# Kernel tuning notes

Measured on AMD Instinct MI355X. Metric: run time of the kernel, lower is better.

## Reference

```python
import jax, jax.numpy as jnp
import numpy as np

N_GAUSS = 1024
IMG = 192
TANFOV = 0.5  # tan(FoV/2), both axes
ZNEAR, ZFAR = 0.01, 100.0

C0 = 0.28209479177387814
C1 = 0.4886025119029199
C2 = (1.0925484305920792, -1.0925484305920792, 0.31539156525252005, -1.0925484305920792, 0.5462742152960396)
C3 = (-0.5900435899266435, 2.890611442640554, -0.4570457994644658, 0.3731763325901154, -0.4570457994644658, 1.445305721320277, -0.5900435899266435)


def _eval_sh3(sh, d):
    # sh: [N,16,3] coeffs, d: [N,3] unit dirs -> clamped rgb [N,3]
    x, y, z = d[:, 0:1], d[:, 1:2], d[:, 2:3]
    xx, yy, zz = x * x, y * y, z * z
    xy, yz, xz = x * y, y * z, x * z
    res = (C0 * sh[:, 0]
           - C1 * y * sh[:, 1] + C1 * z * sh[:, 2] - C1 * x * sh[:, 3]
           + C2[0] * xy * sh[:, 4] + C2[1] * yz * sh[:, 5]
           + C2[2] * (2.0 * zz - xx - yy) * sh[:, 6]
           + C2[3] * xz * sh[:, 7] + C2[4] * (xx - yy) * sh[:, 8]
           + C3[0] * y * (3.0 * xx - yy) * sh[:, 9]
           + C3[1] * xy * z * sh[:, 10]
           + C3[2] * y * (4.0 * zz - xx - yy) * sh[:, 11]
           + C3[3] * z * (2.0 * zz - 3.0 * xx - 3.0 * yy) * sh[:, 12]
           + C3[4] * x * (4.0 * zz - xx - yy) * sh[:, 13]
           + C3[5] * z * (xx - yy) * sh[:, 14]
           + C3[6] * x * (xx - yy - 3.0 * zz) * sh[:, 15])
    return jnp.maximum(res + 0.5, 0.0)


def _quat_to_rot(q):
    r, x, y, z = q[:, 0], q[:, 1], q[:, 2], q[:, 3]
    return jnp.stack([
        1 - 2 * (y * y + z * z), 2 * (x * y - r * z), 2 * (x * z + r * y),
        2 * (x * y + r * z), 1 - 2 * (x * x + z * z), 2 * (y * z - r * x),
        2 * (x * z - r * y), 2 * (y * z + r * x), 1 - 2 * (x * x + y * y),
    ], axis=-1).reshape(-1, 3, 3)


def setup_inputs() -> dict:
    key = jax.random.key(0)
    ks = jax.random.split(key, 6)
    xy = jax.random.uniform(ks[0], (N_GAUSS, 2), minval=-2.0, maxval=2.0)
    z = jax.random.uniform(ks[1], (N_GAUSS, 1), minval=2.0, maxval=10.0)
    means3D = jnp.concatenate([xy, z], axis=1)
    scales = jax.random.uniform(ks[2], (N_GAUSS, 3), minval=0.01, maxval=0.08)
    q = jax.random.normal(ks[3], (N_GAUSS, 4))
    rotations = q / jnp.linalg.norm(q, axis=1, keepdims=True)
    opacities = jax.random.uniform(ks[4], (N_GAUSS, 1), minval=0.1, maxval=0.99)
    shs = jax.random.normal(ks[5], (N_GAUSS, 16, 3)) * 0.3
    viewmatrix = jnp.eye(4, dtype=jnp.float32)
    proj = np.zeros((4, 4), np.float32)
    proj[0, 0] = 1.0 / TANFOV
    proj[1, 1] = 1.0 / TANFOV
    proj[2, 2] = ZFAR / (ZFAR - ZNEAR)
    proj[2, 3] = -ZFAR * ZNEAR / (ZFAR - ZNEAR)
    proj[3, 2] = 1.0
    return dict(means3D=means3D, scales=scales, rotations=rotations,
                opacities=opacities, shs=shs, viewmatrix=viewmatrix,
                projmatrix=jnp.asarray(proj), campos=jnp.zeros(3, jnp.float32),
                bg_color=jnp.zeros(3, jnp.float32),
                image_height=IMG, image_width=IMG)


def reference(means3D, scales, rotations, opacities, shs, viewmatrix,
              projmatrix, campos, bg_color, image_height, image_width):
    H, W = int(image_height), int(image_width)
    fx = W / (2.0 * TANFOV)
    fy = H / (2.0 * TANFOV)
    N = means3D.shape[0]

    # SH -> RGB (convert_SHs_python branch, active_sh_degree = 3)
    dir_pp = means3D - campos[None, :]
    dir_pp = dir_pp / jnp.linalg.norm(dir_pp, axis=1, keepdims=True)
    colors = _eval_sh3(shs, dir_pp)  # [N,3]

    # 3D covariance Sigma = (R S)(R S)^T  (scale_modifier = 1.0)
    R = _quat_to_rot(rotations)
    M = R * scales[:, None, :]
    cov3d = jnp.einsum('nij,nkj->nik', M, M)  # [N,3,3]

    # projection of means
    hom = jnp.concatenate([means3D, jnp.ones((N, 1), means3D.dtype)], axis=1)
    p_view = hom @ viewmatrix.T
    depth = p_view[:, 2]
    p_hom = hom @ projmatrix.T
    p_proj = p_hom[:, :3] / (p_hom[:, 3:4] + 1e-7)
    gx = ((p_proj[:, 0] + 1.0) * W - 1.0) * 0.5  # ndc2Pix
    gy = ((p_proj[:, 1] + 1.0) * H - 1.0) * 0.5
    means2D = jnp.stack([gx, gy], axis=1)

    in_front = depth > 0.2
    tz = jnp.where(in_front, depth, 1.0)
    lim = 1.3 * TANFOV
    tx = jnp.clip(p_view[:, 0] / tz, -lim, lim) * tz
    ty = jnp.clip(p_view[:, 1] / tz, -lim, lim) * tz

    # EWA splatting: J (top 2 rows) composed with view rotation
    zeros = jnp.zeros_like(tz)
    J = jnp.stack([
        jnp.stack([fx / tz, zeros, -fx * tx / (tz * tz)], axis=-1),
        jnp.stack([zeros, fy / tz, -fy * ty / (tz * tz)], axis=-1),
    ], axis=1)  # [N,2,3]
    T = jnp.einsum('nij,jk->nik', J, viewmatrix[:3, :3])
    cov2d = jnp.einsum('nij,njk,nlk->nil', T, cov3d, T)  # [N,2,2]
    a = cov2d[:, 0, 0] + 0.3  # low-pass filter on diagonal
    b = cov2d[:, 0, 1]
    c = cov2d[:, 1, 1] + 0.3

    det = a * c - b * b
    pos_det = det > 0
    inv_det = jnp.where(pos_det, 1.0 / jnp.where(pos_det, det, 1.0), 0.0)
    conA, conB, conC = c * inv_det, -b * inv_det, a * inv_det

    mid = 0.5 * (a + c)
    lam = mid + jnp.sqrt(jnp.maximum(mid * mid - det, 0.1))
    visible = in_front & pos_det
    radii = jnp.where(visible, jnp.ceil(3.0 * jnp.sqrt(lam)), 0.0)
    visibility_filter = radii > 0

    # per-pixel depth-sorted alpha compositing (dense stand-in for tiles)
    yy, xx = jnp.meshgrid(jnp.arange(H, dtype=means3D.dtype),
                          jnp.arange(W, dtype=means3D.dtype), indexing='ij')
    px = xx.reshape(-1)
    py = yy.reshape(-1)
    dx = gx[None, :] - px[:, None]  # [P,N]
    dy = gy[None, :] - py[:, None]
    power = (-0.5 * (conA[None, :] * dx * dx + conC[None, :] * dy * dy)
             - conB[None, :] * dx * dy)
    keep = ((jnp.abs(dx) <= radii[None, :]) & (jnp.abs(dy) <= radii[None, :])
            & visible[None, :] & (power <= 0.0))
    alpha = jnp.minimum(0.99, opacities[:, 0][None, :] * jnp.exp(jnp.minimum(power, 0.0)))
    alpha = jnp.where(keep & (alpha >= 1.0 / 255.0), alpha, 0.0)

    order = jnp.argsort(jnp.where(visible, depth, jnp.inf))
    a_s = alpha[:, order]
    Tcum = jnp.cumprod(1.0 - a_s, axis=1)
    T_before = jnp.concatenate(
        [jnp.ones((a_s.shape[0], 1), a_s.dtype), Tcum[:, :-1]], axis=1)
    wgt = a_s * T_before
    img = wgt @ colors[order] + Tcum[:, -1:] * bg_color[None, :]
    rendered = img.reshape(H, W, 3).transpose(2, 0, 1)  # CHW like torch
    return rendered, radii.astype(jnp.int32), visibility_filter, means2D
```

## Files before the change

### kernel.cpp

```cpp
#include <hip/hip_runtime.h>

#define NG      1024
#define W_IMG   192
#define H_IMG   192
#define HW      (W_IMG * H_IMG)
#define TILES_X 24
#define TILES_Y 24
#define NTILES  (TILES_X * TILES_Y)
#define SMAX    256


__global__ __launch_bounds__(64) void preprocess_kernel(
    const float* __restrict__ means3D, const float* __restrict__ scales,
    const float* __restrict__ rotations, const float* __restrict__ opacities,
    const float* __restrict__ shs, const float* __restrict__ viewm,
    const float* __restrict__ projm, const float* __restrict__ campos,
    float4* __restrict__ pg0, float4* __restrict__ pg1,
    float4* __restrict__ pcol, float* __restrict__ outp)
{
    const int i = blockIdx.x * 64 + threadIdx.x;
    if (i >= NG) return;

    const float mx = means3D[i * 3 + 0];
    const float my = means3D[i * 3 + 1];
    const float mz = means3D[i * 3 + 2];

    float dxc = mx - campos[0], dyc = my - campos[1], dzc = mz - campos[2];
    float nrm = sqrtf(dxc * dxc + dyc * dyc + dzc * dzc);
    float x = dxc / nrm, y = dyc / nrm, z = dzc / nrm;
    float xx = x * x, yy = y * y, zz = z * z;
    float xy = x * y, yz = y * z, xz = x * z;

    float basis[16];
    basis[0]  = 0.28209479177387814f;
    basis[1]  = -0.4886025119029199f * y;
    basis[2]  =  0.4886025119029199f * z;
    basis[3]  = -0.4886025119029199f * x;
    basis[4]  =  1.0925484305920792f * xy;
    basis[5]  = -1.0925484305920792f * yz;
    basis[6]  =  0.31539156525252005f * (2.f * zz - xx - yy);
    basis[7]  = -1.0925484305920792f * xz;
    basis[8]  =  0.5462742152960396f * (xx - yy);
    basis[9]  = -0.5900435899266435f * y * (3.f * xx - yy);
    basis[10] =  2.890611442640554f  * xy * z;
    basis[11] = -0.4570457994644658f * y * (4.f * zz - xx - yy);
    basis[12] =  0.3731763325901154f * z * (2.f * zz - 3.f * xx - 3.f * yy);
    basis[13] = -0.4570457994644658f * x * (4.f * zz - xx - yy);
    basis[14] =  1.445305721320277f  * z * (xx - yy);
    basis[15] = -0.5900435899266435f * x * (xx - yy - 3.f * zz);

    float sh[48];
    const float4* shv = (const float4*)shs + i * 12;
#pragma unroll
    for (int w = 0; w < 12; ++w) {
        float4 q4 = shv[w];
        sh[4 * w + 0] = q4.x; sh[4 * w + 1] = q4.y;
        sh[4 * w + 2] = q4.z; sh[4 * w + 3] = q4.w;
    }
    float cr = 0.f, cg = 0.f, cb = 0.f;
#pragma unroll
    for (int k = 0; k < 16; ++k) {
        float b = basis[k];
        cr += b * sh[3 * k + 0];
        cg += b * sh[3 * k + 1];
        cb += b * sh[3 * k + 2];
    }
    cr = fmaxf(cr + 0.5f, 0.f);
    cg = fmaxf(cg + 0.5f, 0.f);
    cb = fmaxf(cb + 0.5f, 0.f);

    const float4 q = ((const float4*)rotations)[i];
    float qr = q.x, qx = q.y, qy = q.z, qz = q.w;
    float sx = scales[i * 3 + 0], sy = scales[i * 3 + 1], sz = scales[i * 3 + 2];
    float R00 = 1.f - 2.f * (qy * qy + qz * qz), R01 = 2.f * (qx * qy - qr * qz), R02 = 2.f * (qx * qz + qr * qy);
    float R10 = 2.f * (qx * qy + qr * qz), R11 = 1.f - 2.f * (qx * qx + qz * qz), R12 = 2.f * (qy * qz - qr * qx);
    float R20 = 2.f * (qx * qz - qr * qy), R21 = 2.f * (qy * qz + qr * qx), R22 = 1.f - 2.f * (qx * qx + qy * qy);
    float M00 = R00 * sx, M01 = R01 * sy, M02 = R02 * sz;
    float M10 = R10 * sx, M11 = R11 * sy, M12 = R12 * sz;
    float M20 = R20 * sx, M21 = R21 * sy, M22 = R22 * sz;
    float S00 = M00 * M00 + M01 * M01 + M02 * M02;
    float S01 = M00 * M10 + M01 * M11 + M02 * M12;
    float S02 = M00 * M20 + M01 * M21 + M02 * M22;
    float S11 = M10 * M10 + M11 * M11 + M12 * M12;
    float S12 = M10 * M20 + M11 * M21 + M12 * M22;
    float S22 = M20 * M20 + M21 * M21 + M22 * M22;

    float pv0 = viewm[0] * mx + viewm[1] * my + viewm[2]  * mz + viewm[3];
    float pv1 = viewm[4] * mx + viewm[5] * my + viewm[6]  * mz + viewm[7];
    float pv2 = viewm[8] * mx + viewm[9] * my + viewm[10] * mz + viewm[11];
    float ph0 = projm[0]  * mx + projm[1]  * my + projm[2]  * mz + projm[3];
    float ph1 = projm[4]  * mx + projm[5]  * my + projm[6]  * mz + projm[7];
    float ph3 = projm[12] * mx + projm[13] * my + projm[14] * mz + projm[15];
    float pp0 = ph0 / (ph3 + 1e-7f);
    float pp1 = ph1 / (ph3 + 1e-7f);
    float gx = ((pp0 + 1.f) * (float)W_IMG - 1.f) * 0.5f;
    float gy = ((pp1 + 1.f) * (float)H_IMG - 1.f) * 0.5f;

    float depth = pv2;
    bool in_front = depth > 0.2f;
    float tz = in_front ? depth : 1.f;
    const float lim = 1.3f * 0.5f;
    float txv = fminf(fmaxf(pv0 / tz, -lim), lim) * tz;
    float tyv = fminf(fmaxf(pv1 / tz, -lim), lim) * tz;
    const float fx = (float)W_IMG / (2.f * 0.5f);
    const float fy = (float)H_IMG / (2.f * 0.5f);
    float J00 = fx / tz, J02 = -fx * txv / (tz * tz);
    float J11 = fy / tz, J12 = -fy * tyv / (tz * tz);

    float T00 = J00 * viewm[0] + J02 * viewm[8];
    float T01 = J00 * viewm[1] + J02 * viewm[9];
    float T02 = J00 * viewm[2] + J02 * viewm[10];
    float T10 = J11 * viewm[4] + J12 * viewm[8];
    float T11 = J11 * viewm[5] + J12 * viewm[9];
    float T12 = J11 * viewm[6] + J12 * viewm[10];

    float u0 = T00 * S00 + T01 * S01 + T02 * S02;
    float u1 = T00 * S01 + T01 * S11 + T02 * S12;
    float u2 = T00 * S02 + T01 * S12 + T02 * S22;
    float v0 = T10 * S00 + T11 * S01 + T12 * S02;
    float v1 = T10 * S01 + T11 * S11 + T12 * S12;
    float v2 = T10 * S02 + T11 * S12 + T12 * S22;
    float c00 = u0 * T00 + u1 * T01 + u2 * T02;
    float c01 = u0 * T10 + u1 * T11 + u2 * T12;
    float c11 = v0 * T10 + v1 * T11 + v2 * T12;

    float a = c00 + 0.3f;
    float b = c01;
    float c = c11 + 0.3f;
    float det = a * c - b * b;
    bool pos_det = det > 0.f;
    float inv_det = pos_det ? 1.f / det : 0.f;
    float conA = c * inv_det, conB = -b * inv_det, conC = a * inv_det;
    float mid = 0.5f * (a + c);
    float lam = mid + sqrtf(fmaxf(mid * mid - det, 0.1f));
    bool visible = in_front && pos_det;
    float radii = visible ? ceilf(3.f * sqrtf(lam)) : 0.f;

    float opa = opacities[i];

    outp[3 * HW + i]              = radii;
    outp[3 * HW + NG + i]         = (radii > 0.f) ? 1.f : 0.f;
    outp[3 * HW + 2 * NG + 2 * i]     = gx;
    outp[3 * HW + 2 * NG + 2 * i + 1] = gy;

    pg0[i]  = make_float4(gx, gy, radii, visible ? opa : 0.f);
    pg1[i]  = make_float4(conA, conB, conC, depth);
    pcol[i] = make_float4(cr, cg, cb, 0.f);
}

__global__ __launch_bounds__(64) void raster_kernel(
    const float4* __restrict__ pg0, const float4* __restrict__ pg1,
    const float4* __restrict__ pcol, const float* __restrict__ bg,
    float* __restrict__ outp)
{
    __shared__ unsigned int   skey[NG];
    __shared__ unsigned short sgi [NG];
    __shared__ unsigned short ssrt[NG];
    __shared__ float4 sr0[SMAX];
    __shared__ float4 sr1[SMAX];
    __shared__ float4 sc [SMAX];

    const int lane  = threadIdx.x;
    const int tile  = blockIdx.x;
    const int tileX = tile % TILES_X;
    const int tileY = tile / TILES_X;
    const float tx0 = (float)(tileX * 8);
    const float ty0 = (float)(tileY * 8);

    int m = 0;
#pragma unroll 4
    for (int it = 0; it < NG / 64; ++it) {
        const int g = it * 64 + lane;
        float4 g0 = pg0[g];
        bool hit = (g0.w > 0.f) &&
                   (g0.x >= tx0 - g0.z) && (g0.x <= tx0 + 7.f + g0.z) &&
                   (g0.y >= ty0 - g0.z) && (g0.y <= ty0 + 7.f + g0.z);
        unsigned long long mask = __ballot(hit);
        if (hit) {
            int pos = m + __popcll(mask & ((1ULL << lane) - 1ULL));
            float4 g1 = pg1[g];
            skey[pos] = __float_as_uint(g1.w);
            sgi [pos] = (unsigned short)g;
            if (pos < SMAX) {
                sr0[pos] = g0;
                sr1[pos] = g1;
                sc [pos] = pcol[g];
            }
        }
        m += __popcll(mask);
    }
    __syncthreads();

    for (int s = lane; s < m; s += 64) {
        const unsigned int ks = skey[s];
        int rank = 0;
        for (int j = 0; j < m; ++j) {
            unsigned int kj = skey[j];
            rank += (kj < ks || (kj == ks && j < s)) ? 1 : 0;
        }
        ssrt[rank] = (unsigned short)s;
    }
    __syncthreads();

    const int lx = lane & 7, ly = lane >> 3;
    const int pxi = tileX * 8 + lx;
    const int pyi = tileY * 8 + ly;
    const float px = (float)pxi, py = (float)pyi;

    float T = 1.f, accR = 0.f, accG = 0.f, accB = 0.f;
    for (int k = 0; k < m; ++k) {
        const int p = ssrt[k];
        float4 g0, g1, cl;
        if (p < SMAX) {
            g0 = sr0[p]; g1 = sr1[p]; cl = sc[p];
        } else {
            const int gi = sgi[p];
            g0 = pg0[gi]; g1 = pg1[gi]; cl = pcol[gi];
        }
        float dx = g0.x - px, dy = g0.y - py;
        bool cover = (fabsf(dx) <= g0.z) && (fabsf(dy) <= g0.z);
        float power = -0.5f * (g1.x * dx * dx + g1.z * dy * dy) - g1.y * dx * dy;
        float alpha = fminf(0.99f, g0.w * __expf(fminf(power, 0.f)));
        bool keep = cover && (power <= 0.f) && (alpha >= (1.f / 255.f));
        alpha = keep ? alpha : 0.f;
        float w = alpha * T;
        accR += w * cl.x;
        accG += w * cl.y;
        accB += w * cl.z;
        T *= (1.f - alpha);
    }

    const int pix = pyi * W_IMG + pxi;
    outp[pix]          = accR + T * bg[0];
    outp[HW + pix]     = accG + T * bg[1];
    outp[2 * HW + pix] = accB + T * bg[2];
}

extern "C" void kernel_launch(void* const* d_in, const int* in_sizes, int n_in,
                              void* d_out, int out_size, void* d_ws, size_t ws_size,
                              hipStream_t stream)
{
    const float* means3D   = (const float*)d_in[0];
    const float* scales    = (const float*)d_in[1];
    const float* rotations = (const float*)d_in[2];
    const float* opacities = (const float*)d_in[3];
    const float* shs       = (const float*)d_in[4];
    const float* viewm     = (const float*)d_in[5];
    const float* projm     = (const float*)d_in[6];
    const float* campos    = (const float*)d_in[7];
    const float* bg        = (const float*)d_in[8];

    float*  outp = (float*)d_out;
    float4* pg0  = (float4*)d_ws;
    float4* pg1  = pg0 + NG;
    float4* pcol = pg0 + 2 * NG;

    preprocess_kernel<<<NG / 64, 64, 0, stream>>>(
        means3D, scales, rotations, opacities, shs, viewm, projm, campos,
        pg0, pg1, pcol, outp);

    raster_kernel<<<NTILES, 64, 0, stream>>>(pg0, pg1, pcol, bg, outp);
}
```

Before: 91.74 us.

## Split each tile's compositing across four waves and stage all Gaussians in LDS

The raster kernel now runs 512-thread blocks covering two tiles, with four waves per tile. Each block first copies every preprocessed Gaussian into shared memory. Binning uses atomic counters, ranking is split over 256 threads per tile, and the depth-sorted list is divided into four segments that are composited independently and then merged front-to-back. This targets the serial per-tile depth loop and the global-memory fallback reads, at the cost of 48KB+ of LDS per block, lower occupancy, and a redundant full copy of all Gaussians into every block. Ties are now broken by Gaussian index, which keeps the sort order deterministic.

```diff
diff --git a/kernel.cpp b/kernel.cpp
--- a/kernel.cpp
+++ b/kernel.cpp
@@ -7,10 +7,13 @@
 #define TILES_X 24
 #define TILES_Y 24
 #define NTILES  (TILES_X * TILES_Y)
-#define SMAX    256
-
-
-__global__ __launch_bounds__(64) void preprocess_kernel(
+#define TPB     512
+#define TPBK    2
+#define NSEG    4
+#define NBLK    (NTILES / TPBK)
+
+
+__global__ __launch_bounds__(256) void preprocess_kernel(
     const float* __restrict__ means3D, const float* __restrict__ scales,
     const float* __restrict__ rotations, const float* __restrict__ opacities,
     const float* __restrict__ shs, const float* __restrict__ viewm,
@@ -18,7 +21,7 @@
     float4* __restrict__ pg0, float4* __restrict__ pg1,
     float4* __restrict__ pcol, float* __restrict__ outp)
 {
-    const int i = blockIdx.x * 64 + threadIdx.x;
+    const int i = blockIdx.x * 256 + threadIdx.x;
     if (i >= NG) return;
 
     const float mx = means3D[i * 3 + 0];
@@ -148,57 +151,70 @@
     pcol[i] = make_float4(cr, cg, cb, 0.f);
 }
 
-__global__ __launch_bounds__(64) void raster_kernel(
+__global__ __launch_bounds__(TPB) void raster_kernel(
     const float4* __restrict__ pg0, const float4* __restrict__ pg1,
     const float4* __restrict__ pcol, const float* __restrict__ bg,
     float* __restrict__ outp)
 {
-    __shared__ unsigned int   skey[NG];
-    __shared__ unsigned short sgi [NG];
-    __shared__ unsigned short ssrt[NG];
-    __shared__ float4 sr0[SMAX];
-    __shared__ float4 sr1[SMAX];
-    __shared__ float4 sc [SMAX];
-
-    const int lane  = threadIdx.x;
-    const int tile  = blockIdx.x;
+    __shared__ float4 sg0[NG];
+    __shared__ float4 sg1[NG];
+    __shared__ float4 sg2[NG];
+    __shared__ unsigned int   skey[TPBK][NG];
+    __shared__ unsigned short sgi [TPBK][NG];
+    __shared__ unsigned short ssrt[TPBK][NG];
+    __shared__ float4 segacc[TPBK][NSEG * 64];
+    __shared__ int s_cnt[TPBK];
+
+    const int t = threadIdx.x;
+    if (t < TPBK) s_cnt[t] = 0;
+    for (int k = t; k < NG; k += TPB) {
+        sg0[k] = pg0[k];
+        sg1[k] = pg1[k];
+        sg2[k] = pcol[k];
+    }
+    __syncthreads();
+
+    const int wave = t >> 6;
+    const int lane = t & 63;
+    const int tg   = wave >> 2;
+    const int wg   = wave & 3;
+    const int tile = blockIdx.x * TPBK + tg;
     const int tileX = tile % TILES_X;
     const int tileY = tile / TILES_X;
     const float tx0 = (float)(tileX * 8);
     const float ty0 = (float)(tileY * 8);
 
-    int m = 0;
-#pragma unroll 4
-    for (int it = 0; it < NG / 64; ++it) {
-        const int g = it * 64 + lane;
-        float4 g0 = pg0[g];
+#pragma unroll
+    for (int h = 0; h < 4; ++h) {
+        const int g = wg * 256 + h * 64 + lane;
+        float4 g0 = sg0[g];
         bool hit = (g0.w > 0.f) &&
                    (g0.x >= tx0 - g0.z) && (g0.x <= tx0 + 7.f + g0.z) &&
                    (g0.y >= ty0 - g0.z) && (g0.y <= ty0 + 7.f + g0.z);
         unsigned long long mask = __ballot(hit);
+        int base = 0;
+        if (lane == 0 && mask) base = atomicAdd(&s_cnt[tg], __popcll(mask));
+        base = __shfl(base, 0);
         if (hit) {
-            int pos = m + __popcll(mask & ((1ULL << lane) - 1ULL));
-            float4 g1 = pg1[g];
-            skey[pos] = __float_as_uint(g1.w);
-            sgi [pos] = (unsigned short)g;
-            if (pos < SMAX) {
-                sr0[pos] = g0;
-                sr1[pos] = g1;
-                sc [pos] = pcol[g];
-            }
+            int pos = base + __popcll(mask & ((1ULL << lane) - 1ULL));
+            skey[tg][pos] = __float_as_uint(sg1[g].w);
+            sgi [tg][pos] = (unsigned short)g;
         }
-        m += __popcll(mask);
-    }
-    __syncthreads();
-
-    for (int s = lane; s < m; s += 64) {
-        const unsigned int ks = skey[s];
+    }
+    __syncthreads();
+
+    const int m = s_cnt[tg];
+
+    const int lt = wg * 64 + lane;
+    for (int s = lt; s < m; s += 256) {
+        const unsigned int   ks = skey[tg][s];
+        const unsigned short is = sgi[tg][s];
         int rank = 0;
         for (int j = 0; j < m; ++j) {
-            unsigned int kj = skey[j];
-            rank += (kj < ks || (kj == ks && j < s)) ? 1 : 0;
+            unsigned int kj = skey[tg][j];
+            rank += (kj < ks || (kj == ks && sgi[tg][j] < is)) ? 1 : 0;
         }
-        ssrt[rank] = (unsigned short)s;
+        ssrt[tg][rank] = is;
     }
     __syncthreads();
 
@@ -207,16 +223,16 @@
     const int pyi = tileY * 8 + ly;
     const float px = (float)pxi, py = (float)pyi;
 
+    const int chunk = (m + NSEG - 1) / NSEG;
+    const int kbeg = wg * chunk;
+    const int kend = min(m, kbeg + chunk);
+
     float T = 1.f, accR = 0.f, accG = 0.f, accB = 0.f;
-    for (int k = 0; k < m; ++k) {
-        const int p = ssrt[k];
-        float4 g0, g1, cl;
-        if (p < SMAX) {
-            g0 = sr0[p]; g1 = sr1[p]; cl = sc[p];
-        } else {
-            const int gi = sgi[p];
-            g0 = pg0[gi]; g1 = pg1[gi]; cl = pcol[gi];
-        }
+    for (int k = kbeg; k < kend; ++k) {
+        const int gi = ssrt[tg][k];
+        float4 g0 = sg0[gi];
+        float4 g1 = sg1[gi];
+        float4 g2 = sg2[gi];
         float dx = g0.x - px, dy = g0.y - py;
         bool cover = (fabsf(dx) <= g0.z) && (fabsf(dy) <= g0.z);
         float power = -0.5f * (g1.x * dx * dx + g1.z * dy * dy) - g1.y * dx * dy;
@@ -224,16 +240,30 @@
         bool keep = cover && (power <= 0.f) && (alpha >= (1.f / 255.f));
         alpha = keep ? alpha : 0.f;
         float w = alpha * T;
-        accR += w * cl.x;
-        accG += w * cl.y;
-        accB += w * cl.z;
+        accR += w * g2.x;
+        accG += w * g2.y;
+        accB += w * g2.z;
         T *= (1.f - alpha);
     }
 
-    const int pix = pyi * W_IMG + pxi;
-    outp[pix]          = accR + T * bg[0];
-    outp[HW + pix]     = accG + T * bg[1];
-    outp[2 * HW + pix] = accB + T * bg[2];
+    segacc[tg][wg * 64 + lane] = make_float4(accR, accG, accB, T);
+    __syncthreads();
+
+    if (wg == 0) {
+        float Tc = 1.f, r = 0.f, g = 0.f, b = 0.f;
+#pragma unroll
+        for (int s2 = 0; s2 < NSEG; ++s2) {
+            float4 cc = segacc[tg][s2 * 64 + lane];
+            r += Tc * cc.x;
+            g += Tc * cc.y;
+            b += Tc * cc.z;
+            Tc *= cc.w;
+        }
+        const int pix = pyi * W_IMG + pxi;
+        outp[pix]          = r + Tc * bg[0];
+        outp[HW + pix]     = g + Tc * bg[1];
+        outp[2 * HW + pix] = b + Tc * bg[2];
+    }
 }
 
 extern "C" void kernel_launch(void* const* d_in, const int* in_sizes, int n_in,
@@ -255,9 +285,9 @@
     float4* pg1  = pg0 + NG;
     float4* pcol = pg0 + 2 * NG;
 
-    preprocess_kernel<<<NG / 64, 64, 0, stream>>>(
+    preprocess_kernel<<<NG / 256, 256, 0, stream>>>(
         means3D, scales, rotations, opacities, shs, viewm, projm, campos,
         pg0, pg1, pcol, outp);
 
-    raster_kernel<<<NTILES, 64, 0, stream>>>(pg0, pg1, pcol, bg, outp);
+    raster_kernel<<<NBLK, TPB, 0, stream>>>(pg0, pg1, pcol, bg, outp);
 }
```

Result: faster. 84.38 us (-8.0%).

## Split per-tile compositing across four waves and merge segment transmittances

Applied to the files above, without the earlier changes.

The raster kernel grows from one wave to four waves per 8x8 tile. Culling is parallelised with a shared atomic counter, and the O(m^2) rank sort is spread across 256 threads using a combined 64-bit depth+index key, which removes the tie-break branch. Each wave composites a contiguous depth segment, and wave 0 merges the segments through their accumulated colour and transmittance. This raises parallelism across the 576 tiles at the cost of more shared memory, extra syncs, and a different floating-point association order in the blend. Because the atomic makes culled-list order nondeterministic, the SMAX cache now holds an arbitrary subset, though the sort stays deterministic.

```diff
diff --git a/kernel.cpp b/kernel.cpp
--- a/kernel.cpp
+++ b/kernel.cpp
@@ -7,7 +7,8 @@
 #define TILES_X 24
 #define TILES_Y 24
 #define NTILES  (TILES_X * TILES_Y)
-#define SMAX    256
+#define NSEG    4
+#define SMAX    384
 
 
 __global__ __launch_bounds__(64) void preprocess_kernel(
@@ -148,56 +149,63 @@
     pcol[i] = make_float4(cr, cg, cb, 0.f);
 }
 
-__global__ __launch_bounds__(64) void raster_kernel(
+__global__ __launch_bounds__(256) void raster_kernel(
     const float4* __restrict__ pg0, const float4* __restrict__ pg1,
     const float4* __restrict__ pcol, const float* __restrict__ bg,
     float* __restrict__ outp)
 {
-    __shared__ unsigned int   skey[NG];
-    __shared__ unsigned short sgi [NG];
-    __shared__ unsigned short ssrt[NG];
+    __shared__ unsigned long long skey[NG];
+    __shared__ unsigned short     ssrt[NG];
     __shared__ float4 sr0[SMAX];
     __shared__ float4 sr1[SMAX];
     __shared__ float4 sc [SMAX];
-
-    const int lane  = threadIdx.x;
-    const int tile  = blockIdx.x;
+    __shared__ float4 segacc[NSEG * 64];
+    __shared__ int s_cnt;
+
+    const int t    = threadIdx.x;
+    const int wave = t >> 6;
+    const int lane = t & 63;
+    const int tile = blockIdx.x;
     const int tileX = tile % TILES_X;
     const int tileY = tile / TILES_X;
     const float tx0 = (float)(tileX * 8);
     const float ty0 = (float)(tileY * 8);
 
-    int m = 0;
-#pragma unroll 4
-    for (int it = 0; it < NG / 64; ++it) {
-        const int g = it * 64 + lane;
+    if (t == 0) s_cnt = 0;
+    __syncthreads();
+
+#pragma unroll
+    for (int h = 0; h < NG / 256; ++h) {
+        const int g = h * 256 + t;
         float4 g0 = pg0[g];
         bool hit = (g0.w > 0.f) &&
                    (g0.x >= tx0 - g0.z) && (g0.x <= tx0 + 7.f + g0.z) &&
                    (g0.y >= ty0 - g0.z) && (g0.y <= ty0 + 7.f + g0.z);
         unsigned long long mask = __ballot(hit);
+        int base = 0;
+        if (lane == 0 && mask) base = atomicAdd(&s_cnt, __popcll(mask));
+        base = __shfl(base, 0);
         if (hit) {
-            int pos = m + __popcll(mask & ((1ULL << lane) - 1ULL));
+            int pos = base + __popcll(mask & ((1ULL << lane) - 1ULL));
             float4 g1 = pg1[g];
-            skey[pos] = __float_as_uint(g1.w);
-            sgi [pos] = (unsigned short)g;
+            skey[pos] = ((unsigned long long)__float_as_uint(g1.w) << 16)
+                        | (unsigned)g;
             if (pos < SMAX) {
                 sr0[pos] = g0;
                 sr1[pos] = g1;
                 sc [pos] = pcol[g];
             }
         }
-        m += __popcll(mask);
-    }
-    __syncthreads();
-
-    for (int s = lane; s < m; s += 64) {
-        const unsigned int ks = skey[s];
+    }
+    __syncthreads();
+
+    const int m = s_cnt;
+
+    for (int s = t; s < m; s += 256) {
+        const unsigned long long ks = skey[s];
         int rank = 0;
-        for (int j = 0; j < m; ++j) {
-            unsigned int kj = skey[j];
-            rank += (kj < ks || (kj == ks && j < s)) ? 1 : 0;
-        }
+        for (int j = 0; j < m; ++j)
+            rank += (skey[j] < ks) ? 1 : 0;
         ssrt[rank] = (unsigned short)s;
     }
     __syncthreads();
@@ -207,14 +215,18 @@
     const int pyi = tileY * 8 + ly;
     const float px = (float)pxi, py = (float)pyi;
 
+    const int chunk = (m + NSEG - 1) / NSEG;
+    const int kbeg = wave * chunk;
+    const int kend = min(m, kbeg + chunk);
+
     float T = 1.f, accR = 0.f, accG = 0.f, accB = 0.f;
-    for (int k = 0; k < m; ++k) {
+    for (int k = kbeg; k < kend; ++k) {
         const int p = ssrt[k];
         float4 g0, g1, cl;
         if (p < SMAX) {
             g0 = sr0[p]; g1 = sr1[p]; cl = sc[p];
         } else {
-            const int gi = sgi[p];
+            const int gi = (int)(skey[p] & 0xFFFFu);
             g0 = pg0[gi]; g1 = pg1[gi]; cl = pcol[gi];
         }
         float dx = g0.x - px, dy = g0.y - py;
@@ -230,10 +242,24 @@
         T *= (1.f - alpha);
     }
 
-    const int pix = pyi * W_IMG + pxi;
-    outp[pix]          = accR + T * bg[0];
-    outp[HW + pix]     = accG + T * bg[1];
-    outp[2 * HW + pix] = accB + T * bg[2];
+    segacc[wave * 64 + lane] = make_float4(accR, accG, accB, T);
+    __syncthreads();
+
+    if (wave == 0) {
+        float Tc = 1.f, r = 0.f, g = 0.f, b = 0.f;
+#pragma unroll
+        for (int s2 = 0; s2 < NSEG; ++s2) {
+            float4 cc = segacc[s2 * 64 + lane];
+            r += Tc * cc.x;
+            g += Tc * cc.y;
+            b += Tc * cc.z;
+            Tc *= cc.w;
+        }
+        const int pix = pyi * W_IMG + pxi;
+        outp[pix]          = r + Tc * bg[0];
+        outp[HW + pix]     = g + Tc * bg[1];
+        outp[2 * HW + pix] = b + Tc * bg[2];
+    }
 }
 
 extern "C" void kernel_launch(void* const* d_in, const int* in_sizes, int n_in,
@@ -259,5 +285,5 @@
         means3D, scales, rotations, opacities, shs, viewm, projm, campos,
         pg0, pg1, pcol, outp);
 
-    raster_kernel<<<NTILES, 64, 0, stream>>>(pg0, pg1, pcol, bg, outp);
+    raster_kernel<<<NTILES, 256, 0, stream>>>(pg0, pg1, pcol, bg, outp);
 }
```

Measured after the change: 82.24 us. 10.4% less time.
